# Kernel optimization log

Measured on AMD Instinct MI355X. Metric: run time of the kernel, lower is better.

The kernel has to match this reference:

```python
import jax, jax.numpy as jnp
import numpy as np

IN_DIM = 4096
OUT_DIM = 4096
CODEBOOK_SIZE = 65536
LAYER_ID = 3
HASH_A, HASH_B, HASH_C = 10007, 20011, 40009
SIGN_HASH_A, SIGN_HASH_B, SIGN_HASH_C = 4099, 6151, 14887
SIGNED_HASH = True
BATCH = 8192


def _hash_tables():
    i = jnp.arange(OUT_DIM, dtype=jnp.int64 if jax.config.jax_enable_x64 else jnp.int32)[:, None]
    j = jnp.arange(IN_DIM, dtype=i.dtype)[None, :]
    idx = (i * HASH_A + j * HASH_B + LAYER_ID * HASH_C) % CODEBOOK_SIZE
    bits = (i * SIGN_HASH_A + j * SIGN_HASH_B + LAYER_ID * SIGN_HASH_C) % 2
    signs = bits.astype(jnp.float32) * 2.0 - 1.0
    return idx, signs


def setup_inputs() -> dict:
    key = jax.random.key(0)
    kx, kc = jax.random.split(key)
    x = jax.random.normal(kx, (BATCH, IN_DIM), dtype=jnp.float32)
    codebook = jax.random.normal(kc, (CODEBOOK_SIZE,), dtype=jnp.float32) * 0.01
    bias = jnp.zeros((OUT_DIM,), dtype=jnp.float32)
    return {"x": x, "codebook": codebook, "bias": bias}


def reference(x, codebook, bias):
    idx, signs = _hash_tables()  # [out_dim, in_dim] each
    weight = codebook[idx]  # gather from tiny codebook -> [out_dim, in_dim]
    if SIGNED_HASH:
        weight = weight * signs.astype(weight.dtype)
    # F.linear: y = x @ W^T + b
    return jnp.einsum('bi,oi->bo', x, weight) + bias
```

## Files before the change

### kernel.cpp

```cpp
#include <hip/hip_runtime.h>
#include <hip/hip_bf16.h>

constexpr int M_ = 8192;
constexpr int N_ = 4096;
constexpr int K_ = 4096;
constexpr int CBOOK = 65536;
constexpr int HA = 10007, HB = 20011;
constexpr int HC3 = 3 * 40009;

constexpr int BM = 128, BN = 128, BK = 32;

using bf16x8 = __bf16 __attribute__((ext_vector_type(8)));
using f32x4  = float __attribute__((ext_vector_type(4)));
using u16x8  = unsigned short __attribute__((ext_vector_type(8)));

typedef __attribute__((address_space(3))) void lds_void_t;
typedef const __attribute__((address_space(1))) void gbl_void_t;

static __device__ __forceinline__ unsigned short f2bf(float f) {
    __bf16 h = (__bf16)f;
    return __builtin_bit_cast(unsigned short, h);
}

__global__ __launch_bounds__(256) void gen_w_kernel(const float* __restrict__ cb,
                                                    unsigned short* __restrict__ W) {
    const int t  = blockIdx.x * 256 + threadIdx.x;
    const int o  = t >> 9;
    const int ib = (t & 511) << 3;
    const int h  = o * HA + ib * HB + HC3;
    u16x8 out;
#pragma unroll
    for (int j = 0; j < 8; ++j) {
        const int idx = (h + j * HB) & (CBOOK - 1);
        float v = cb[idx];
        v = ((o ^ (ib + j)) & 1) ? -v : v;
        out[j] = f2bf(v);
    }
    *reinterpret_cast<u16x8*>(&W[(size_t)o * K_ + ib]) = out;
}

__global__ __launch_bounds__(256) void conv_x_kernel(const float* __restrict__ x,
                                                     unsigned short* __restrict__ xb) {
    const size_t t = (size_t)blockIdx.x * 256 + threadIdx.x;
    const float4* p = reinterpret_cast<const float4*>(x) + t * 2;
    const float4 a = p[0], b = p[1];
    u16x8 out;
    out[0] = f2bf(a.x); out[1] = f2bf(a.y); out[2] = f2bf(a.z); out[3] = f2bf(a.w);
    out[4] = f2bf(b.x); out[5] = f2bf(b.y); out[6] = f2bf(b.z); out[7] = f2bf(b.w);
    reinterpret_cast<u16x8*>(xb)[t] = out;
}

template <bool PRECONV>
__global__ __launch_bounds__(256) void gemm_kernel(const void* __restrict__ Asrc,
                                                   const unsigned short* __restrict__ W,
                                                   const float* __restrict__ bias,
                                                   float* __restrict__ C) {
    __shared__ __align__(16) unsigned short ldsA[BM * BK];
    __shared__ __align__(16) unsigned short ldsB[BN * BK];

    const int tid  = threadIdx.x;
    const int lane = tid & 63;
    const int wv   = tid >> 6;
    const int wm   = wv >> 1;
    const int wn   = wv & 1;
    const int m0 = blockIdx.y * BM;
    const int n0 = blockIdx.x * BN;

    const int quad = lane >> 4;
    const int l16  = lane & 15;

    f32x4 acc[4][4] = {};

    for (int k0 = 0; k0 < K_; k0 += BK) {
        {
            const unsigned short* gB = W + (size_t)n0 * K_ + k0;
#pragma unroll
            for (int r = 0; r < 2; ++r) {
                const int rowb = r * 64 + wv * 16;
                const unsigned short* src =
                    gB + (size_t)(rowb + (lane >> 2)) * K_ + (lane & 3) * 8;
                __builtin_amdgcn_global_load_lds((gbl_void_t*)src,
                                                 (lds_void_t*)&ldsB[rowb * BK], 16, 0, 0);
            }
        }
        if constexpr (PRECONV) {
            const unsigned short* gA =
                (const unsigned short*)Asrc + (size_t)m0 * K_ + k0;
#pragma unroll
            for (int r = 0; r < 2; ++r) {
                const int rowb = r * 64 + wv * 16;
                const unsigned short* src =
                    gA + (size_t)(rowb + (lane >> 2)) * K_ + (lane & 3) * 8;
                __builtin_amdgcn_global_load_lds((gbl_void_t*)src,
                                                 (lds_void_t*)&ldsA[rowb * BK], 16, 0, 0);
            }
        } else {
            const float* xf = (const float*)Asrc;
            const int arow = tid >> 1;
            const int acol = (tid & 1) * 16;
            const float4* src = reinterpret_cast<const float4*>(
                xf + (size_t)(m0 + arow) * K_ + k0 + acol);
            const float4 v0 = src[0], v1 = src[1], v2 = src[2], v3 = src[3];
            u16x8 o0, o1;
            o0[0] = f2bf(v0.x); o0[1] = f2bf(v0.y); o0[2] = f2bf(v0.z); o0[3] = f2bf(v0.w);
            o0[4] = f2bf(v1.x); o0[5] = f2bf(v1.y); o0[6] = f2bf(v1.z); o0[7] = f2bf(v1.w);
            o1[0] = f2bf(v2.x); o1[1] = f2bf(v2.y); o1[2] = f2bf(v2.z); o1[3] = f2bf(v2.w);
            o1[4] = f2bf(v3.x); o1[5] = f2bf(v3.y); o1[6] = f2bf(v3.z); o1[7] = f2bf(v3.w);
            *reinterpret_cast<u16x8*>(&ldsA[arow * BK + acol]) = o0;
            *reinterpret_cast<u16x8*>(&ldsA[arow * BK + acol + 8]) = o1;
        }
        __syncthreads();

        bf16x8 af[4], bfr[4];
        const int ka = quad * 8;
#pragma unroll
        for (int mt = 0; mt < 4; ++mt)
            af[mt] = *reinterpret_cast<const bf16x8*>(
                &ldsA[(wm * 64 + mt * 16 + l16) * BK + ka]);
#pragma unroll
        for (int nt = 0; nt < 4; ++nt)
            bfr[nt] = *reinterpret_cast<const bf16x8*>(
                &ldsB[(wn * 64 + nt * 16 + l16) * BK + ka]);
#pragma unroll
        for (int mt = 0; mt < 4; ++mt)
#pragma unroll
            for (int nt = 0; nt < 4; ++nt)
                acc[mt][nt] = __builtin_amdgcn_mfma_f32_16x16x32_bf16(
                    af[mt], bfr[nt], acc[mt][nt], 0, 0, 0);

        __syncthreads();
    }

#pragma unroll
    for (int nt = 0; nt < 4; ++nt) {
        const int col = n0 + wn * 64 + nt * 16 + l16;
        const float bv = bias[col];
#pragma unroll
        for (int mt = 0; mt < 4; ++mt) {
            const int rowb = m0 + wm * 64 + mt * 16 + quad * 4;
#pragma unroll
            for (int r = 0; r < 4; ++r)
                C[(size_t)(rowb + r) * N_ + col] = acc[mt][nt][r] + bv;
        }
    }
}

__global__ __launch_bounds__(256) void naive_kernel(const float* __restrict__ x,
                                                    const float* __restrict__ cb,
                                                    const float* __restrict__ bias,
                                                    float* __restrict__ out) {
    const size_t t = (size_t)blockIdx.x * 256 + threadIdx.x;
    const int row = (int)(t / N_);
    const int col = (int)(t % N_);
    float s = bias[col];
    const float* xr = x + (size_t)row * K_;
    const int h = col * HA + HC3;
    for (int i = 0; i < K_; ++i) {
        float v = cb[(h + i * HB) & (CBOOK - 1)];
        s += xr[i] * (((col ^ i) & 1) ? -v : v);
    }
    out[t] = s;
}

extern "C" void kernel_launch(void* const* d_in, const int* in_sizes, int n_in,
                              void* d_out, int out_size, void* d_ws, size_t ws_size,
                              hipStream_t stream) {
    const float* x    = (const float*)d_in[0];
    const float* cb   = (const float*)d_in[1];
    const float* bias = (const float*)d_in[2];
    float* out = (float*)d_out;

    const size_t wBytes = (size_t)N_ * K_ * sizeof(unsigned short);
    const size_t xBytes = (size_t)M_ * K_ * sizeof(unsigned short);

    if (ws_size >= wBytes + xBytes) {
        unsigned short* W  = (unsigned short*)d_ws;
        unsigned short* xb = (unsigned short*)((char*)d_ws + wBytes);
        gen_w_kernel<<<N_ * K_ / 8 / 256, 256, 0, stream>>>(cb, W);
        conv_x_kernel<<<M_ * K_ / 8 / 256, 256, 0, stream>>>(x, xb);
        gemm_kernel<true><<<dim3(N_ / BN, M_ / BM), 256, 0, stream>>>(
            (const void*)xb, W, bias, out);
    } else if (ws_size >= wBytes) {
        unsigned short* W = (unsigned short*)d_ws;
        gen_w_kernel<<<N_ * K_ / 8 / 256, 256, 0, stream>>>(cb, W);
        gemm_kernel<false><<<dim3(N_ / BN, M_ / BM), 256, 0, stream>>>(
            (const void*)x, W, bias, out);
    } else {
        naive_kernel<<<(int)((size_t)M_ * N_ / 256), 256, 0, stream>>>(x, cb, bias, out);
    }
}
```

Baseline: 549.6 us.

## Double GEMM K-tile, add XOR-swizzled LDS layout, and merge prep kernels

```diff
diff --git a/kernel.cpp b/kernel.cpp
--- a/kernel.cpp
+++ b/kernel.cpp
@@ -8,7 +8,7 @@
 constexpr int HA = 10007, HB = 20011;
 constexpr int HC3 = 3 * 40009;
 
-constexpr int BM = 128, BN = 128, BK = 32;
+constexpr int BM = 128, BN = 128, BK = 64;
 
 using bf16x8 = __bf16 __attribute__((ext_vector_type(8)));
 using f32x4  = float __attribute__((ext_vector_type(4)));
@@ -22,36 +22,40 @@
     return __builtin_bit_cast(unsigned short, h);
 }
 
-__global__ __launch_bounds__(256) void gen_w_kernel(const float* __restrict__ cb,
-                                                    unsigned short* __restrict__ W) {
-    const int t  = blockIdx.x * 256 + threadIdx.x;
-    const int o  = t >> 9;
-    const int ib = (t & 511) << 3;
-    const int h  = o * HA + ib * HB + HC3;
-    u16x8 out;
+constexpr int GENB  = N_ * K_ / 8 / 256;
+constexpr int CONVB = M_ * K_ / 8 / 256;
+
+__global__ __launch_bounds__(256) void prep_kernel(const float* __restrict__ x,
+                                                   const float* __restrict__ cb,
+                                                   unsigned short* __restrict__ W,
+                                                   unsigned short* __restrict__ xb) {
+    const int b = blockIdx.x;
+    if (b < GENB) {
+        const int t  = b * 256 + threadIdx.x;
+        const int o  = t >> 9;
+        const int ib = (t & 511) << 3;
+        const int h  = o * HA + ib * HB + HC3;
+        u16x8 out;
 #pragma unroll
-    for (int j = 0; j < 8; ++j) {
-        const int idx = (h + j * HB) & (CBOOK - 1);
-        float v = cb[idx];
-        v = ((o ^ (ib + j)) & 1) ? -v : v;
-        out[j] = f2bf(v);
+        for (int j = 0; j < 8; ++j) {
+            const int idx = (h + j * HB) & (CBOOK - 1);
+            float v = cb[idx];
+            v = ((o ^ (ib + j)) & 1) ? -v : v;
+            out[j] = f2bf(v);
+        }
+        *reinterpret_cast<u16x8*>(&W[(size_t)o * K_ + ib]) = out;
+    } else {
+        const size_t t = (size_t)(b - GENB) * 256 + threadIdx.x;
+        const float4* p = reinterpret_cast<const float4*>(x) + t * 2;
+        const float4 a = p[0], c = p[1];
+        u16x8 out;
+        out[0] = f2bf(a.x); out[1] = f2bf(a.y); out[2] = f2bf(a.z); out[3] = f2bf(a.w);
+        out[4] = f2bf(c.x); out[5] = f2bf(c.y); out[6] = f2bf(c.z); out[7] = f2bf(c.w);
+        reinterpret_cast<u16x8*>(xb)[t] = out;
     }
-    *reinterpret_cast<u16x8*>(&W[(size_t)o * K_ + ib]) = out;
 }
 
-__global__ __launch_bounds__(256) void conv_x_kernel(const float* __restrict__ x,
-                                                     unsigned short* __restrict__ xb) {
-    const size_t t = (size_t)blockIdx.x * 256 + threadIdx.x;
-    const float4* p = reinterpret_cast<const float4*>(x) + t * 2;
-    const float4 a = p[0], b = p[1];
-    u16x8 out;
-    out[0] = f2bf(a.x); out[1] = f2bf(a.y); out[2] = f2bf(a.z); out[3] = f2bf(a.w);
-    out[4] = f2bf(b.x); out[5] = f2bf(b.y); out[6] = f2bf(b.z); out[7] = f2bf(b.w);
-    reinterpret_cast<u16x8*>(xb)[t] = out;
-}
-
-template <bool PRECONV>
-__global__ __launch_bounds__(256) void gemm_kernel(const void* __restrict__ Asrc,
+__global__ __launch_bounds__(256) void gemm_kernel(const unsigned short* __restrict__ A,
                                                    const unsigned short* __restrict__ W,
                                                    const float* __restrict__ bias,
                                                    float* __restrict__ C) {
@@ -68,66 +72,49 @@
 
     const int quad = lane >> 4;
     const int l16  = lane & 15;
+    const int lr = lane >> 3;
+    const int lc = lane & 7;
+    const int scol = (lc ^ lr) * 8;
+    const int sw   = l16 & 7;
 
     f32x4 acc[4][4] = {};
 
     for (int k0 = 0; k0 < K_; k0 += BK) {
         {
+            const unsigned short* gA = A + (size_t)m0 * K_ + k0;
             const unsigned short* gB = W + (size_t)n0 * K_ + k0;
 #pragma unroll
-            for (int r = 0; r < 2; ++r) {
-                const int rowb = r * 64 + wv * 16;
-                const unsigned short* src =
-                    gB + (size_t)(rowb + (lane >> 2)) * K_ + (lane & 3) * 8;
-                __builtin_amdgcn_global_load_lds((gbl_void_t*)src,
+            for (int r = 0; r < 4; ++r) {
+                const int rowb = wv * 32 + r * 8;
+                const unsigned short* srcA = gA + (size_t)(rowb + lr) * K_ + scol;
+                const unsigned short* srcB = gB + (size_t)(rowb + lr) * K_ + scol;
+                __builtin_amdgcn_global_load_lds((gbl_void_t*)srcA,
+                                                 (lds_void_t*)&ldsA[rowb * BK], 16, 0, 0);
+                __builtin_amdgcn_global_load_lds((gbl_void_t*)srcB,
                                                  (lds_void_t*)&ldsB[rowb * BK], 16, 0, 0);
             }
         }
-        if constexpr (PRECONV) {
-            const unsigned short* gA =
-                (const unsigned short*)Asrc + (size_t)m0 * K_ + k0;
-#pragma unroll
-            for (int r = 0; r < 2; ++r) {
-                const int rowb = r * 64 + wv * 16;
-                const unsigned short* src =
-                    gA + (size_t)(rowb + (lane >> 2)) * K_ + (lane & 3) * 8;
-                __builtin_amdgcn_global_load_lds((gbl_void_t*)src,
-                                                 (lds_void_t*)&ldsA[rowb * BK], 16, 0, 0);
-            }
-        } else {
-            const float* xf = (const float*)Asrc;
-            const int arow = tid >> 1;
-            const int acol = (tid & 1) * 16;
-            const float4* src = reinterpret_cast<const float4*>(
-                xf + (size_t)(m0 + arow) * K_ + k0 + acol);
-            const float4 v0 = src[0], v1 = src[1], v2 = src[2], v3 = src[3];
-            u16x8 o0, o1;
-            o0[0] = f2bf(v0.x); o0[1] = f2bf(v0.y); o0[2] = f2bf(v0.z); o0[3] = f2bf(v0.w);
-            o0[4] = f2bf(v1.x); o0[5] = f2bf(v1.y); o0[6] = f2bf(v1.z); o0[7] = f2bf(v1.w);
-            o1[0] = f2bf(v2.x); o1[1] = f2bf(v2.y); o1[2] = f2bf(v2.z); o1[3] = f2bf(v2.w);
-            o1[4] = f2bf(v3.x); o1[5] = f2bf(v3.y); o1[6] = f2bf(v3.z); o1[7] = f2bf(v3.w);
-            *reinterpret_cast<u16x8*>(&ldsA[arow * BK + acol]) = o0;
-            *reinterpret_cast<u16x8*>(&ldsA[arow * BK + acol + 8]) = o1;
-        }
         __syncthreads();
 
-        bf16x8 af[4], bfr[4];
-        const int ka = quad * 8;
 #pragma unroll
-        for (int mt = 0; mt < 4; ++mt)
-            af[mt] = *reinterpret_cast<const bf16x8*>(
-                &ldsA[(wm * 64 + mt * 16 + l16) * BK + ka]);
+        for (int kk = 0; kk < 2; ++kk) {
+            bf16x8 af[4], bfr[4];
+            const int blk = ((kk * 4 + quad) ^ sw) * 8;
 #pragma unroll
-        for (int nt = 0; nt < 4; ++nt)
-            bfr[nt] = *reinterpret_cast<const bf16x8*>(
-                &ldsB[(wn * 64 + nt * 16 + l16) * BK + ka]);
-#pragma unroll
-        for (int mt = 0; mt < 4; ++mt)
+            for (int mt = 0; mt < 4; ++mt)
+                af[mt] = *reinterpret_cast<const bf16x8*>(
+                    &ldsA[(wm * 64 + mt * 16 + l16) * BK + blk]);
 #pragma unroll
             for (int nt = 0; nt < 4; ++nt)
-                acc[mt][nt] = __builtin_amdgcn_mfma_f32_16x16x32_bf16(
-                    af[mt], bfr[nt], acc[mt][nt], 0, 0, 0);
-
+                bfr[nt] = *reinterpret_cast<const bf16x8*>(
+                    &ldsB[(wn * 64 + nt * 16 + l16) * BK + blk]);
+#pragma unroll
+            for (int mt = 0; mt < 4; ++mt)
+#pragma unroll
+                for (int nt = 0; nt < 4; ++nt)
+                    acc[mt][nt] = __builtin_amdgcn_mfma_f32_16x16x32_bf16(
+                        af[mt], bfr[nt], acc[mt][nt], 0, 0, 0);
+        }
         __syncthreads();
     }
 
@@ -176,15 +163,8 @@
     if (ws_size >= wBytes + xBytes) {
         unsigned short* W  = (unsigned short*)d_ws;
         unsigned short* xb = (unsigned short*)((char*)d_ws + wBytes);
-        gen_w_kernel<<<N_ * K_ / 8 / 256, 256, 0, stream>>>(cb, W);
-        conv_x_kernel<<<M_ * K_ / 8 / 256, 256, 0, stream>>>(x, xb);
-        gemm_kernel<true><<<dim3(N_ / BN, M_ / BM), 256, 0, stream>>>(
-            (const void*)xb, W, bias, out);
-    } else if (ws_size >= wBytes) {
-        unsigned short* W = (unsigned short*)d_ws;
-        gen_w_kernel<<<N_ * K_ / 8 / 256, 256, 0, stream>>>(cb, W);
-        gemm_kernel<false><<<dim3(N_ / BN, M_ / BM), 256, 0, stream>>>(
-            (const void*)x, W, bias, out);
+        prep_kernel<<<GENB + CONVB, 256, 0, stream>>>(x, cb, W, xb);
+        gemm_kernel<<<dim3(N_ / BN, M_ / BM), 256, 0, stream>>>(xb, W, bias, out);
     } else {
         naive_kernel<<<(int)((size_t)M_ * N_ / 256), 256, 0, stream>>>(x, cb, bias, out);
     }
```

New measurement: 542.7 us. About the same (-1.3%).
